# Kernel optimization log

Hardware: AMD Instinct MI355X
Metric: run time of the kernel (lower is better)

## Reference

```python
import jax, jax.numpy as jnp
import numpy as np

B = 128
N_ATOMS = 4096
NB, NA, NT = 4095, 4094, 4093
MAX_LEN = 5 * NT  # 20465, longest packed column (torsions)
EPS = 1e-8


def setup_inputs() -> dict:
    key = jax.random.key(0)
    ks = jax.random.split(key, 24)
    feats = jnp.zeros((B, MAX_LEN, 9), jnp.float32)
    # col 0: atom type ids
    atoms = jax.random.randint(ks[0], (B, N_ATOMS), 0, 6)
    # col 5: coords, flattened (N_ATOMS, 3)
    coords = jax.random.normal(ks[1], (B, N_ATOMS, 3), jnp.float32) * 5.0
    # col 6: bonds (i, j, type)
    bonds = jnp.stack([
        jax.random.randint(ks[2], (B, NB), 0, N_ATOMS),
        jax.random.randint(ks[3], (B, NB), 0, N_ATOMS),
        jax.random.randint(ks[4], (B, NB), 0, 15)], axis=-1)
    # col 7: angles (i, j, k, type)
    angles = jnp.stack([
        jax.random.randint(ks[5], (B, NA), 0, N_ATOMS),
        jax.random.randint(ks[6], (B, NA), 0, N_ATOMS),
        jax.random.randint(ks[7], (B, NA), 0, N_ATOMS),
        jax.random.randint(ks[8], (B, NA), 0, 13)], axis=-1)
    # col 8: torsions (i, j, k, l, type)
    tors = jnp.stack([
        jax.random.randint(ks[9], (B, NT), 0, N_ATOMS),
        jax.random.randint(ks[10], (B, NT), 0, N_ATOMS),
        jax.random.randint(ks[11], (B, NT), 0, N_ATOMS),
        jax.random.randint(ks[12], (B, NT), 0, N_ATOMS),
        jax.random.randint(ks[13], (B, NT), 0, 25)], axis=-1)
    feats = feats.at[:, :N_ATOMS, 0].set(atoms.astype(jnp.float32))
    feats = feats.at[:, :3 * N_ATOMS, 5].set(coords.reshape(B, -1))
    feats = feats.at[:, :3 * NB, 6].set(bonds.reshape(B, -1).astype(jnp.float32))
    feats = feats.at[:, :4 * NA, 7].set(angles.reshape(B, -1).astype(jnp.float32))
    feats = feats.at[:, :5 * NT, 8].set(tors.reshape(B, -1).astype(jnp.float32))
    lengths = jnp.tile(jnp.array(
        [[N_ATOMS, 0, 0, 0, 0, 3 * N_ATOMS, 3 * NB, 4 * NA, 5 * NT]],
        jnp.int32), (B, 1))
    bond_type = jnp.stack([jnp.ones(15), jax.random.uniform(ks[14], (15,), minval=1.0, maxval=2.0)], -1).astype(jnp.float32)
    angle_type = jnp.stack([jnp.ones(13), jax.random.uniform(ks[15], (13,), minval=1.0, maxval=3.0)], -1).astype(jnp.float32)
    tor_type = jnp.stack([jnp.ones(25), jax.random.uniform(ks[16], (25,), minval=0.0, maxval=3.14)], -1).astype(jnp.float32)
    multiplicity = jax.random.randint(ks[17], (25,), 1, 4)
    opt_pars = jax.random.uniform(ks[18], (47,), minval=0.5, maxval=1.5).astype(jnp.float32)
    return {"features": feats, "lengths": lengths, "bond_type": bond_type,
            "angle_type": angle_type, "tor_type": tor_type,
            "multiplicity": multiplicity, "opt_pars": opt_pars}


def _sample_energy(f, bond_type, angle_type, tor_type, multiplicity, opt_pars):
    coords = f[:3 * N_ATOMS, 5].reshape(-1, 3)                      # [N,3]
    bonds = f[:3 * NB, 6].astype(jnp.int32).reshape(-1, 3)          # [NB,3]
    angles = f[:4 * NA, 7].astype(jnp.int32).reshape(-1, 4)         # [NA,4]
    tors = f[:5 * NT, 8].astype(jnp.int32).reshape(-1, 5)           # [NT,5]

    # bonds: harmonic k*(r - r0)^2
    d = coords[bonds[:, 0]] - coords[bonds[:, 1]]
    r = jnp.sqrt(jnp.sum(d * d, -1) + EPS)
    pb = bond_type[bonds[:, 2]]
    e_bond = opt_pars[0] * jnp.sum(pb[:, 0] * (r - pb[:, 1]) ** 2)

    # angles: harmonic k*(theta - theta0)^2
    v1 = coords[angles[:, 0]] - coords[angles[:, 1]]
    v2 = coords[angles[:, 2]] - coords[angles[:, 1]]
    cosang = jnp.sum(v1 * v2, -1) / (
        jnp.sqrt(jnp.sum(v1 * v1, -1) + EPS) * jnp.sqrt(jnp.sum(v2 * v2, -1) + EPS))
    theta = jnp.arccos(jnp.clip(cosang, -1.0 + 1e-6, 1.0 - 1e-6))
    pa = angle_type[angles[:, 3]]
    e_ang = opt_pars[1] * jnp.sum(pa[:, 0] * (theta - pa[:, 1]) ** 2)

    # torsions: periodic k*(1 + cos(n*phi - delta))
    ci, cj, ck, cl = (coords[tors[:, m]] for m in range(4))
    b1, b2, b3 = cj - ci, ck - cj, cl - ck
    n1 = jnp.cross(b1, b2)
    n2 = jnp.cross(b2, b3)
    b2n = b2 / jnp.sqrt(jnp.sum(b2 * b2, -1, keepdims=True) + EPS)
    m1 = jnp.cross(n1, b2n)
    phi = jnp.arctan2(jnp.sum(m1 * n2, -1), jnp.sum(n1 * n2, -1))
    pt = tor_type[tors[:, 4]]
    n_mult = multiplicity[tors[:, 4]].astype(jnp.float32)
    e_tor = opt_pars[2] * jnp.sum(pt[:, 0] * (1.0 + jnp.cos(n_mult * phi - pt[:, 1])))

    return jnp.stack([e_bond, e_ang, e_tor])


def reference(features, lengths, bond_type, angle_type, tor_type, multiplicity, opt_pars):
    # lengths are uniform across batch (constants above); vmap over batch dim
    return jax.vmap(_sample_energy, in_axes=(0, None, None, None, None, None))(
        features, bond_type, angle_type, tor_type, multiplicity, opt_pars)
```

## Files before the change

### kernel.cpp

```cpp
#include <hip/hip_runtime.h>
#include <math.h>

#define BATCH    128
#define N_ATOMS  4096
#define NB       4095
#define NA       4094
#define NT       4093
#define FSTRIDE  184185
#define ROWS     20465
#define CROWS    12288
#define BROWS    12285
#define AROWS    16376
#define EPSV     1e-8f
#define THREADS  1024
#define WAVES    16
#define TPR      120

typedef float float4a __attribute__((ext_vector_type(4), aligned(4)));

__global__ __launch_bounds__(THREADS, 1) void
local_energy_v11(const float* __restrict__ F,
                 const float* __restrict__ bond_type,
                 const float* __restrict__ angle_type,
                 const float* __restrict__ tor_type,
                 const int*   __restrict__ multiplicity,
                 const float* __restrict__ opt_pars,
                 float*       __restrict__ out)
{
    __shared__ float          scc[CROWS];
    __shared__ unsigned short sbB[BROWS + 1];
    __shared__ unsigned short sbA[AROWS];
    __shared__ unsigned short sbT[ROWS + 1];
    __shared__ float sbt[30], sat[26], stt[50], smu[25];
    __shared__ float sred[WAVES * 2];

    const int b   = blockIdx.x;
    const int x   = b & 7;
    const int g   = b >> 3;
    const int s   = (g & 15) * 8 + x;
    const int p   = g >> 4;
    const int tid = threadIdx.x;
    const int w   = tid >> 6;
    const int l   = tid & 63;
    const size_t sbase = (size_t)s * FSTRIDE;

    if (tid < 30)                      sbt[tid]       = bond_type[tid];
    else if (tid >= 32 && tid < 58)    sat[tid - 32]  = angle_type[tid - 32];
    else if (tid >= 64 && tid < 114)   stt[tid - 64]  = tor_type[tid - 64];
    else if (tid >= 128 && tid < 153)  smu[tid - 128] = (float)multiplicity[tid - 128];

    const int tmax = p ? 137 : 171;
    for (int t = w; t < tmax; t += WAVES) {
        const int R0 = TPR * t + 2 * l;
        const int R1 = R0 + 1;
        float4a v0, v1;
        const bool ok0 = (R0 < ROWS);
        const bool ok1 = (R1 < ROWS);
        if (ok0) v0 = *(const float4a*)(F + sbase + (size_t)9 * R0 + 5);
        if (ok1) v1 = *(const float4a*)(F + sbase + (size_t)9 * R1 + 5);

        if (R1 < CROWS) {
            float2 c2; c2.x = v0.x; c2.y = v1.x;
            *(float2*)(scc + R0) = c2;
        }
        if (p) {
            if (R1 < BROWS) {
                unsigned pk = (unsigned)(unsigned short)(int)v0.y
                            | ((unsigned)(unsigned short)(int)v1.y << 16);
                *(unsigned*)(sbB + R0) = pk;
            } else if (R0 < BROWS) {
                sbB[R0] = (unsigned short)(int)v0.y;
            }
            if (R1 < AROWS) {
                unsigned pk = (unsigned)(unsigned short)(int)v0.z
                            | ((unsigned)(unsigned short)(int)v1.z << 16);
                *(unsigned*)(sbA + R0) = pk;
            }
        } else {
            if (ok1) {
                unsigned pk = (unsigned)(unsigned short)(int)v0.w
                            | ((unsigned)(unsigned short)(int)v1.w << 16);
                *(unsigned*)(sbT + R0) = pk;
            } else if (ok0) {
                sbT[R0] = (unsigned short)(int)v0.w;
            }
        }
    }
    __syncthreads();

    float eA = 0.f, eB = 0.f;
    if (p) {
        for (int i = tid; i < NB; i += THREADS) {
            const int a0 = sbB[3 * i + 0];
            const int a1 = sbB[3 * i + 1];
            const int bt = sbB[3 * i + 2];
            const float dx = scc[3 * a0 + 0] - scc[3 * a1 + 0];
            const float dy = scc[3 * a0 + 1] - scc[3 * a1 + 1];
            const float dz = scc[3 * a0 + 2] - scc[3 * a1 + 2];
            const float r  = sqrtf(dx * dx + dy * dy + dz * dz + EPSV);
            const float t0 = r - sbt[bt * 2 + 1];
            eA += sbt[bt * 2 + 0] * t0 * t0;
        }
        for (int i = tid; i < NA; i += THREADS) {
            const int a0 = sbA[4 * i + 0];
            const int a1 = sbA[4 * i + 1];
            const int a2 = sbA[4 * i + 2];
            const int at = sbA[4 * i + 3];
            const float v1x = scc[3 * a0 + 0] - scc[3 * a1 + 0];
            const float v1y = scc[3 * a0 + 1] - scc[3 * a1 + 1];
            const float v1z = scc[3 * a0 + 2] - scc[3 * a1 + 2];
            const float v2x = scc[3 * a2 + 0] - scc[3 * a1 + 0];
            const float v2y = scc[3 * a2 + 1] - scc[3 * a1 + 1];
            const float v2z = scc[3 * a2 + 2] - scc[3 * a1 + 2];
            const float d12 = v1x * v2x + v1y * v2y + v1z * v2z;
            const float n1  = sqrtf(v1x * v1x + v1y * v1y + v1z * v1z + EPSV);
            const float n2  = sqrtf(v2x * v2x + v2y * v2y + v2z * v2z + EPSV);
            float cosang = d12 / (n1 * n2);
            cosang = fminf(fmaxf(cosang, -1.0f + 1e-6f), 1.0f - 1e-6f);
            const float t0 = acosf(cosang) - sat[at * 2 + 1];
            eB += sat[at * 2 + 0] * t0 * t0;
        }
    } else {
        for (int i = tid; i < NT; i += THREADS) {
            const int ai = sbT[5 * i + 0];
            const int aj = sbT[5 * i + 1];
            const int ak = sbT[5 * i + 2];
            const int al = sbT[5 * i + 3];
            const int tt = sbT[5 * i + 4];
            const float b1x = scc[3*aj+0] - scc[3*ai+0];
            const float b1y = scc[3*aj+1] - scc[3*ai+1];
            const float b1z = scc[3*aj+2] - scc[3*ai+2];
            const float b2x = scc[3*ak+0] - scc[3*aj+0];
            const float b2y = scc[3*ak+1] - scc[3*aj+1];
            const float b2z = scc[3*ak+2] - scc[3*aj+2];
            const float b3x = scc[3*al+0] - scc[3*ak+0];
            const float b3y = scc[3*al+1] - scc[3*ak+1];
            const float b3z = scc[3*al+2] - scc[3*ak+2];
            const float n1x = b1y*b2z - b1z*b2y;
            const float n1y = b1z*b2x - b1x*b2z;
            const float n1z = b1x*b2y - b1y*b2x;
            const float n2x = b2y*b3z - b2z*b3y;
            const float n2y = b2z*b3x - b2x*b3z;
            const float n2z = b2x*b3y - b2y*b3x;
            const float inv = 1.0f / sqrtf(b2x*b2x + b2y*b2y + b2z*b2z + EPSV);
            const float bnx = b2x * inv, bny = b2y * inv, bnz = b2z * inv;
            const float m1x = n1y*bnz - n1z*bny;
            const float m1y = n1z*bnx - n1x*bnz;
            const float m1z = n1x*bny - n1y*bnx;
            const float phi = atan2f(m1x*n2x + m1y*n2y + m1z*n2z,
                                     n1x*n2x + n1y*n2y + n1z*n2z);
            eA += stt[tt * 2 + 0] * (1.0f + cosf(smu[tt] * phi - stt[tt * 2 + 1]));
        }
    }

    for (int off = 32; off > 0; off >>= 1) {
        eA += __shfl_down(eA, off);
        eB += __shfl_down(eB, off);
    }
    if (l == 0) {
        sred[w * 2 + 0] = eA;
        sred[w * 2 + 1] = eB;
    }
    __syncthreads();
    if (tid == 0) {
        float rA = 0.f, rB = 0.f;
        for (int i = 0; i < WAVES; ++i) { rA += sred[i * 2]; rB += sred[i * 2 + 1]; }
        if (p) {
            out[s * 3 + 0] = opt_pars[0] * rA;
            out[s * 3 + 1] = opt_pars[1] * rB;
        } else {
            out[s * 3 + 2] = opt_pars[2] * rA;
        }
    }
}

extern "C" void kernel_launch(void* const* d_in, const int* in_sizes, int n_in,
                              void* d_out, int out_size, void* d_ws, size_t ws_size,
                              hipStream_t stream) {
    const float* F            = (const float*)d_in[0];
    const float* bond_type    = (const float*)d_in[2];
    const float* angle_type   = (const float*)d_in[3];
    const float* tor_type     = (const float*)d_in[4];
    const int*   multiplicity = (const int*)  d_in[5];
    const float* opt_pars     = (const float*)d_in[6];
    float* out = (float*)d_out;

    local_energy_v11<<<dim3(BATCH * 2), dim3(THREADS), 0, stream>>>(
        F, bond_type, angle_type, tor_type, multiplicity, opt_pars, out);
}
```

Measured before the change: 154.1 us.

## Split feature loading between block pairs and exchange via workspace with grid sync

Adds a cooperative kernel in which each pair of blocks per sample loads a disjoint half of the sample's packed feature rows. The loads are contiguous, coalesced float4 chunks rather than the strided per-row reads used before. Each block scatters its columns into LDS, writes the part its partner needs to a global workspace, syncs the whole grid, and reads the partner's data back before computing bond/angle or torsion energies. This removes the duplicated read of coordinates and the strided access pattern, at the cost of a grid-wide barrier, an extra global round trip, and a dependence on the cooperative launch and workspace being available, with the old kernel kept as a fallback.

```diff
diff --git a/kernel.cpp b/kernel.cpp
--- a/kernel.cpp
+++ b/kernel.cpp
@@ -1,5 +1,8 @@
 #include <hip/hip_runtime.h>
+#include <hip/hip_cooperative_groups.h>
 #include <math.h>
+
+namespace cg = cooperative_groups;
 
 #define BATCH    128
 #define N_ATOMS  4096
@@ -16,7 +19,254 @@
 #define WAVES    16
 #define TPR      120
 
+#define NCHUNK_FULL 46046
+#define HCHUNK      23023
+#define SPLIT_ROW   10232
+
+#define OFF_SCC  0
+#define OFF_B    49152
+#define OFF_A    73728
+#define OFF_T    106480
+#define OFF_SBT  147412
+#define OFF_SAT  147532
+#define OFF_STT  147636
+#define OFF_SMU  147836
+#define OFF_SRED 147936
+#define OFF_D4   148128
+#define OFF_D2   148132
+#define LDS_SZ   148160
+
+#define WC       0
+#define WT       12288
+#define WB       17404
+#define WA       18432
+#define WSLOT    21504
+#define WS_NEED  ((size_t)WSLOT * 4 * BATCH)
+
 typedef float float4a __attribute__((ext_vector_type(4), aligned(4)));
+
+
+__device__ __forceinline__ float sel4f(const float4a v, const int e) {
+    float r = v.w;
+    r = (e == 0) ? v.x : r;
+    r = (e == 1) ? v.y : r;
+    r = (e == 2) ? v.z : r;
+    return r;
+}
+
+__device__ __forceinline__ void extract_chunk(char* __restrict__ lds,
+                                              const float4a v,
+                                              const int r0, const int c0) {
+    {
+        const float cv = sel4f(v, 5 - c0);
+        const bool  ok = ((unsigned)(5 - c0) < 4u) && (r0 < CROWS);
+        const int   ad = ok ? (OFF_SCC + (r0 << 2)) : OFF_D4;
+        *(float*)(lds + ad) = cv;
+    }
+    {
+        const int  iv = (int)sel4f(v, 6 - c0);
+        const bool ok = ((unsigned)(6 - c0) < 4u) && (r0 < BROWS);
+        const int  ad = ok ? (OFF_B + (r0 << 1)) : OFF_D2;
+        *(unsigned short*)(lds + ad) = (unsigned short)iv;
+    }
+    {
+        const int  iv = (int)sel4f(v, 7 - c0);
+        const bool ok = ((unsigned)(7 - c0) < 4u) && (r0 < AROWS);
+        const int  ad = ok ? (OFF_A + (r0 << 1)) : OFF_D2;
+        *(unsigned short*)(lds + ad) = (unsigned short)iv;
+    }
+    {
+        const int  iv = (int)sel4f(v, 8 - c0);
+        const bool ok = ((unsigned)(8 - c0) < 4u);
+        const int  ad = ok ? (OFF_T + (r0 << 1)) : OFF_D2;
+        *(unsigned short*)(lds + ad) = (unsigned short)iv;
+    }
+}
+
+__global__ __launch_bounds__(THREADS, 1) void
+local_energy_v16(const float* __restrict__ F,
+                 const float* __restrict__ bond_type,
+                 const float* __restrict__ angle_type,
+                 const float* __restrict__ tor_type,
+                 const int*   __restrict__ multiplicity,
+                 const float* __restrict__ opt_pars,
+                 unsigned*    __restrict__ ws,
+                 float*       __restrict__ out)
+{
+    __shared__ __align__(16) char LDSM[LDS_SZ];
+    char* lds = LDSM;
+
+    const int b   = blockIdx.x;
+    const int s   = b >> 1;
+    const int h   = b & 1;
+    const int tid = threadIdx.x;
+    const int w   = tid >> 6;
+    const int l   = tid & 63;
+    const float* Fb = F + (size_t)s * FSTRIDE;
+
+    float* sbt = (float*)(lds + OFF_SBT);
+    float* sat = (float*)(lds + OFF_SAT);
+    float* stt = (float*)(lds + OFF_STT);
+    float* smu = (float*)(lds + OFF_SMU);
+    float* srd = (float*)(lds + OFF_SRED);
+
+    if (tid < 30)                      sbt[tid]       = bond_type[tid];
+    else if (tid >= 32 && tid < 58)    sat[tid - 32]  = angle_type[tid - 32];
+    else if (tid >= 64 && tid < 114)   stt[tid - 64]  = tor_type[tid - 64];
+    else if (tid >= 128 && tid < 153)  smu[tid - 128] = (float)multiplicity[tid - 128];
+
+    const int cbase = h ? HCHUNK : 0;
+    {
+        const int f0i = 4 * (cbase + tid);
+        int r0 = f0i / 9;
+        int c0 = f0i - 9 * r0;
+
+        for (int j = 0; j < 22; j += 2) {
+            const int ci0 = cbase + tid + (j << 10);
+            const float4a v0 = *(const float4a*)(Fb + 4 * ci0);
+            const float4a v1 = *(const float4a*)(Fb + 4 * ci0 + 4096);
+            extract_chunk(lds, v0, r0, c0);
+            { c0 += 1; r0 += 455; if (c0 == 9) { c0 = 0; r0 += 1; } }
+            extract_chunk(lds, v1, r0, c0);
+            { c0 += 1; r0 += 455; if (c0 == 9) { c0 = 0; r0 += 1; } }
+        }
+        if (tid < 495) {
+            const int ci = cbase + tid + (22 << 10);
+            const float4a v = *(const float4a*)(Fb + 4 * ci);
+            extract_chunk(lds, v, r0, c0);
+        } else if (h && tid == 495) {
+            const float x = Fb[FSTRIDE - 1];
+            *(unsigned short*)(lds + OFF_T + (20464 << 1)) = (unsigned short)(int)x;
+        }
+    }
+    __syncthreads();
+
+    unsigned* W = ws + (size_t)s * WSLOT;
+    if (h == 0) {
+        const unsigned* sC = (const unsigned*)(lds + OFF_SCC);
+        for (int i = tid; i < 10232; i += THREADS) W[WC + i] = sC[i];
+        const unsigned* sT = (const unsigned*)(lds + OFF_T);
+        for (int i = tid; i < 5116; i += THREADS) W[WT + i] = sT[i];
+    } else {
+        const unsigned* sC = (const unsigned*)(lds + OFF_SCC);
+        for (int i = tid; i < 2056; i += THREADS) W[WC + SPLIT_ROW + i] = sC[SPLIT_ROW + i];
+        const unsigned* sB = (const unsigned*)(lds + OFF_B);
+        for (int i = tid; i < 1027; i += THREADS) W[WB + i] = sB[5116 + i];
+        const unsigned* sA = (const unsigned*)(lds + OFF_A);
+        for (int i = tid; i < 3072; i += THREADS) W[WA + i] = sA[5116 + i];
+    }
+
+    __threadfence();
+    cg::this_grid().sync();
+    __threadfence();
+
+    if (h == 0) {
+        unsigned* dC = (unsigned*)(lds + OFF_SCC);
+        for (int i = tid; i < 2056; i += THREADS) dC[SPLIT_ROW + i] = W[WC + SPLIT_ROW + i];
+        unsigned* dB = (unsigned*)(lds + OFF_B);
+        for (int i = tid; i < 1027; i += THREADS) dB[5116 + i] = W[WB + i];
+        unsigned* dA = (unsigned*)(lds + OFF_A);
+        for (int i = tid; i < 3072; i += THREADS) dA[5116 + i] = W[WA + i];
+    } else {
+        unsigned* dC = (unsigned*)(lds + OFF_SCC);
+        for (int i = tid; i < 10232; i += THREADS) dC[i] = W[WC + i];
+        unsigned* dT = (unsigned*)(lds + OFF_T);
+        for (int i = tid; i < 5116; i += THREADS) dT[i] = W[WT + i];
+    }
+    __syncthreads();
+
+    const float*          scc = (const float*)(lds + OFF_SCC);
+    const unsigned short* pB  = (const unsigned short*)(lds + OFF_B);
+    const unsigned short* pA  = (const unsigned short*)(lds + OFF_A);
+    const unsigned short* pT  = (const unsigned short*)(lds + OFF_T);
+
+    float eA = 0.f, eB = 0.f;
+    if (h == 0) {
+        for (int i = tid; i < NB; i += THREADS) {
+            const int a0 = pB[3 * i + 0];
+            const int a1 = pB[3 * i + 1];
+            const int bt = pB[3 * i + 2];
+            const float dx = scc[3 * a0 + 0] - scc[3 * a1 + 0];
+            const float dy = scc[3 * a0 + 1] - scc[3 * a1 + 1];
+            const float dz = scc[3 * a0 + 2] - scc[3 * a1 + 2];
+            const float r  = sqrtf(dx * dx + dy * dy + dz * dz + EPSV);
+            const float t0 = r - sbt[bt * 2 + 1];
+            eA += sbt[bt * 2 + 0] * t0 * t0;
+        }
+        for (int i = tid; i < NA; i += THREADS) {
+            const int a0 = pA[4 * i + 0];
+            const int a1 = pA[4 * i + 1];
+            const int a2 = pA[4 * i + 2];
+            const int at = pA[4 * i + 3];
+            const float v1x = scc[3 * a0 + 0] - scc[3 * a1 + 0];
+            const float v1y = scc[3 * a0 + 1] - scc[3 * a1 + 1];
+            const float v1z = scc[3 * a0 + 2] - scc[3 * a1 + 2];
+            const float v2x = scc[3 * a2 + 0] - scc[3 * a1 + 0];
+            const float v2y = scc[3 * a2 + 1] - scc[3 * a1 + 1];
+            const float v2z = scc[3 * a2 + 2] - scc[3 * a1 + 2];
+            const float d12 = v1x * v2x + v1y * v2y + v1z * v2z;
+            const float n1  = sqrtf(v1x * v1x + v1y * v1y + v1z * v1z + EPSV);
+            const float n2  = sqrtf(v2x * v2x + v2y * v2y + v2z * v2z + EPSV);
+            float cosang = d12 / (n1 * n2);
+            cosang = fminf(fmaxf(cosang, -1.0f + 1e-6f), 1.0f - 1e-6f);
+            const float t0 = acosf(cosang) - sat[at * 2 + 1];
+            eB += sat[at * 2 + 0] * t0 * t0;
+        }
+    } else {
+        for (int i = tid; i < NT; i += THREADS) {
+            const int ai = pT[5 * i + 0];
+            const int aj = pT[5 * i + 1];
+            const int ak = pT[5 * i + 2];
+            const int al = pT[5 * i + 3];
+            const int tt = pT[5 * i + 4];
+            const float b1x = scc[3*aj+0] - scc[3*ai+0];
+            const float b1y = scc[3*aj+1] - scc[3*ai+1];
+            const float b1z = scc[3*aj+2] - scc[3*ai+2];
+            const float b2x = scc[3*ak+0] - scc[3*aj+0];
+            const float b2y = scc[3*ak+1] - scc[3*aj+1];
+            const float b2z = scc[3*ak+2] - scc[3*aj+2];
+            const float b3x = scc[3*al+0] - scc[3*ak+0];
+            const float b3y = scc[3*al+1] - scc[3*ak+1];
+            const float b3z = scc[3*al+2] - scc[3*ak+2];
+            const float n1x = b1y*b2z - b1z*b2y;
+            const float n1y = b1z*b2x - b1x*b2z;
+            const float n1z = b1x*b2y - b1y*b2x;
+            const float n2x = b2y*b3z - b2z*b3y;
+            const float n2y = b2z*b3x - b2x*b3z;
+            const float n2z = b2x*b3y - b2y*b3x;
+            const float inv = 1.0f / sqrtf(b2x*b2x + b2y*b2y + b2z*b2z + EPSV);
+            const float bnx = b2x * inv, bny = b2y * inv, bnz = b2z * inv;
+            const float m1x = n1y*bnz - n1z*bny;
+            const float m1y = n1z*bnx - n1x*bnz;
+            const float m1z = n1x*bny - n1y*bnx;
+            const float phi = atan2f(m1x*n2x + m1y*n2y + m1z*n2z,
+                                     n1x*n2x + n1y*n2y + n1z*n2z);
+            eA += stt[tt * 2 + 0] * (1.0f + cosf(smu[tt] * phi - stt[tt * 2 + 1]));
+        }
+    }
+
+    for (int off = 32; off > 0; off >>= 1) {
+        eA += __shfl_down(eA, off);
+        eB += __shfl_down(eB, off);
+    }
+    if (l == 0) {
+        srd[w * 2 + 0] = eA;
+        srd[w * 2 + 1] = eB;
+    }
+    __syncthreads();
+    if (tid == 0) {
+        float rA = 0.f, rB = 0.f;
+        for (int i = 0; i < WAVES; ++i) { rA += srd[i * 2]; rB += srd[i * 2 + 1]; }
+        if (h == 0) {
+            out[s * 3 + 0] = opt_pars[0] * rA;
+            out[s * 3 + 1] = opt_pars[1] * rB;
+        } else {
+            out[s * 3 + 2] = opt_pars[2] * rA;
+        }
+    }
+}
+
+typedef float float4f __attribute__((ext_vector_type(4), aligned(4)));
 
 __global__ __launch_bounds__(THREADS, 1) void
 local_energy_v11(const float* __restrict__ F,
@@ -53,12 +303,11 @@
     for (int t = w; t < tmax; t += WAVES) {
         const int R0 = TPR * t + 2 * l;
         const int R1 = R0 + 1;
-        float4a v0, v1;
+        float4f v0, v1;
         const bool ok0 = (R0 < ROWS);
         const bool ok1 = (R1 < ROWS);
-        if (ok0) v0 = *(const float4a*)(F + sbase + (size_t)9 * R0 + 5);
-        if (ok1) v1 = *(const float4a*)(F + sbase + (size_t)9 * R1 + 5);
-
+        if (ok0) v0 = *(const float4f*)(F + sbase + (size_t)9 * R0 + 5);
+        if (ok1) v1 = *(const float4f*)(F + sbase + (size_t)9 * R1 + 5);
         if (R1 < CROWS) {
             float2 c2; c2.x = v0.x; c2.y = v1.x;
             *(float2*)(scc + R0) = c2;
@@ -183,8 +432,19 @@
     const float* tor_type     = (const float*)d_in[4];
     const int*   multiplicity = (const int*)  d_in[5];
     const float* opt_pars     = (const float*)d_in[6];
-    float* out = (float*)d_out;
-
+    float*       out          = (float*)d_out;
+    unsigned*    wsp          = (unsigned*)d_ws;
+
+    if (d_ws != nullptr && ws_size >= WS_NEED) {
+        void* args[] = { (void*)&F, (void*)&bond_type, (void*)&angle_type,
+                         (void*)&tor_type, (void*)&multiplicity,
+                         (void*)&opt_pars, (void*)&wsp, (void*)&out };
+        hipError_t e = hipLaunchCooperativeKernel(
+            reinterpret_cast<void*>(local_energy_v16),
+            dim3(BATCH * 2), dim3(THREADS), args, 0, stream);
+        if (e == hipSuccess) return;
+        (void)hipGetLastError();
+    }
     local_energy_v11<<<dim3(BATCH * 2), dim3(THREADS), 0, stream>>>(
         F, bond_type, angle_type, tor_type, multiplicity, opt_pars, out);
 }
```

Result: slower. 347.7 us (+125.7%).

## Overlap bond and torsion compute with tail of global staging loads

Applied to the files above, without the earlier changes.

Splits the staging loop into a head phase that loads coordinates and the early index rows, then a tail phase. During the tail, global loads for the remaining angle or torsion rows are issued while already-staged bonds and the first torsions are evaluated. The aim is to hide global memory latency behind compute instead of serialising load then compute. It adds an extra barrier and relies on hard-coded cut points (HEAD_T, CUT_T) being consistent with which rows are already in shared memory.

```diff
diff --git a/kernel.cpp b/kernel.cpp
--- a/kernel.cpp
+++ b/kernel.cpp
@@ -15,11 +15,66 @@
 #define THREADS  1024
 #define WAVES    16
 #define TPR      120
+#define HEAD_T   103
+#define CUT_T    2472
 
 typedef float float4a __attribute__((ext_vector_type(4), aligned(4)));
 
+
+__device__ __forceinline__ float bond_term(const int i,
+        const unsigned short* __restrict__ sbB,
+        const float* __restrict__ scc,
+        const float* __restrict__ sbt)
+{
+    const int a0 = sbB[3 * i + 0];
+    const int a1 = sbB[3 * i + 1];
+    const int bt = sbB[3 * i + 2];
+    const float dx = scc[3 * a0 + 0] - scc[3 * a1 + 0];
+    const float dy = scc[3 * a0 + 1] - scc[3 * a1 + 1];
+    const float dz = scc[3 * a0 + 2] - scc[3 * a1 + 2];
+    const float r  = sqrtf(dx * dx + dy * dy + dz * dz + EPSV);
+    const float t0 = r - sbt[bt * 2 + 1];
+    return sbt[bt * 2 + 0] * t0 * t0;
+}
+
+__device__ __forceinline__ float tor_term(const int i,
+        const unsigned short* __restrict__ sbT,
+        const float* __restrict__ scc,
+        const float* __restrict__ stt,
+        const float* __restrict__ smu)
+{
+    const int ai = sbT[5 * i + 0];
+    const int aj = sbT[5 * i + 1];
+    const int ak = sbT[5 * i + 2];
+    const int al = sbT[5 * i + 3];
+    const int tt = sbT[5 * i + 4];
+    const float b1x = scc[3*aj+0] - scc[3*ai+0];
+    const float b1y = scc[3*aj+1] - scc[3*ai+1];
+    const float b1z = scc[3*aj+2] - scc[3*ai+2];
+    const float b2x = scc[3*ak+0] - scc[3*aj+0];
+    const float b2y = scc[3*ak+1] - scc[3*aj+1];
+    const float b2z = scc[3*ak+2] - scc[3*aj+2];
+    const float b3x = scc[3*al+0] - scc[3*ak+0];
+    const float b3y = scc[3*al+1] - scc[3*ak+1];
+    const float b3z = scc[3*al+2] - scc[3*ak+2];
+    const float n1x = b1y*b2z - b1z*b2y;
+    const float n1y = b1z*b2x - b1x*b2z;
+    const float n1z = b1x*b2y - b1y*b2x;
+    const float n2x = b2y*b3z - b2z*b3y;
+    const float n2y = b2z*b3x - b2x*b3z;
+    const float n2z = b2x*b3y - b2y*b3x;
+    const float inv = 1.0f / sqrtf(b2x*b2x + b2y*b2y + b2z*b2z + EPSV);
+    const float bnx = b2x * inv, bny = b2y * inv, bnz = b2z * inv;
+    const float m1x = n1y*bnz - n1z*bny;
+    const float m1y = n1z*bnx - n1x*bnz;
+    const float m1z = n1x*bny - n1y*bnx;
+    const float phi = atan2f(m1x*n2x + m1y*n2y + m1z*n2z,
+                             n1x*n2x + n1y*n2y + n1z*n2z);
+    return stt[tt * 2 + 0] * (1.0f + cosf(smu[tt] * phi - stt[tt * 2 + 1]));
+}
+
 __global__ __launch_bounds__(THREADS, 1) void
-local_energy_v11(const float* __restrict__ F,
+local_energy_v17(const float* __restrict__ F,
                  const float* __restrict__ bond_type,
                  const float* __restrict__ angle_type,
                  const float* __restrict__ tor_type,
@@ -49,15 +104,13 @@
     else if (tid >= 64 && tid < 114)   stt[tid - 64]  = tor_type[tid - 64];
     else if (tid >= 128 && tid < 153)  smu[tid - 128] = (float)multiplicity[tid - 128];
 
-    const int tmax = p ? 137 : 171;
-    for (int t = w; t < tmax; t += WAVES) {
+    float eA = 0.f, eB = 0.f;
+
+    for (int t = w; t < HEAD_T; t += WAVES) {
         const int R0 = TPR * t + 2 * l;
         const int R1 = R0 + 1;
-        float4a v0, v1;
-        const bool ok0 = (R0 < ROWS);
-        const bool ok1 = (R1 < ROWS);
-        if (ok0) v0 = *(const float4a*)(F + sbase + (size_t)9 * R0 + 5);
-        if (ok1) v1 = *(const float4a*)(F + sbase + (size_t)9 * R1 + 5);
+        const float4a v0 = *(const float4a*)(F + sbase + (size_t)9 * R0 + 5);
+        const float4a v1 = *(const float4a*)(F + sbase + (size_t)9 * R1 + 5);
 
         if (R1 < CROWS) {
             float2 c2; c2.x = v0.x; c2.y = v1.x;
@@ -71,36 +124,46 @@
             } else if (R0 < BROWS) {
                 sbB[R0] = (unsigned short)(int)v0.y;
             }
+            {
+                unsigned pk = (unsigned)(unsigned short)(int)v0.z
+                            | ((unsigned)(unsigned short)(int)v1.z << 16);
+                *(unsigned*)(sbA + R0) = pk;
+            }
+        } else {
+            {
+                unsigned pk = (unsigned)(unsigned short)(int)v0.w
+                            | ((unsigned)(unsigned short)(int)v1.w << 16);
+                *(unsigned*)(sbT + R0) = pk;
+            }
+        }
+    }
+    __syncthreads();
+
+    if (p) {
+        int q = 0;
+        for (int t = HEAD_T + w; t < 137; t += WAVES) {
+            const int R0 = TPR * t + 2 * l;
+            const int R1 = R0 + 1;
+            const float4a v0 = *(const float4a*)(F + sbase + (size_t)9 * R0 + 5);
+            const float4a v1 = *(const float4a*)(F + sbase + (size_t)9 * R1 + 5);
+
+            if (q == 0) {
+                eA += bond_term(tid, sbB, scc, sbt);
+                eA += bond_term(tid + 1024, sbB, scc, sbt);
+            } else if (q == 1) {
+                eA += bond_term(tid + 2048, sbB, scc, sbt);
+                if (tid + 3072 < NB) eA += bond_term(tid + 3072, sbB, scc, sbt);
+            }
+            ++q;
+
             if (R1 < AROWS) {
                 unsigned pk = (unsigned)(unsigned short)(int)v0.z
                             | ((unsigned)(unsigned short)(int)v1.z << 16);
                 *(unsigned*)(sbA + R0) = pk;
             }
-        } else {
-            if (ok1) {
-                unsigned pk = (unsigned)(unsigned short)(int)v0.w
-                            | ((unsigned)(unsigned short)(int)v1.w << 16);
-                *(unsigned*)(sbT + R0) = pk;
-            } else if (ok0) {
-                sbT[R0] = (unsigned short)(int)v0.w;
-            }
-        }
-    }
-    __syncthreads();
-
-    float eA = 0.f, eB = 0.f;
-    if (p) {
-        for (int i = tid; i < NB; i += THREADS) {
-            const int a0 = sbB[3 * i + 0];
-            const int a1 = sbB[3 * i + 1];
-            const int bt = sbB[3 * i + 2];
-            const float dx = scc[3 * a0 + 0] - scc[3 * a1 + 0];
-            const float dy = scc[3 * a0 + 1] - scc[3 * a1 + 1];
-            const float dz = scc[3 * a0 + 2] - scc[3 * a1 + 2];
-            const float r  = sqrtf(dx * dx + dy * dy + dz * dz + EPSV);
-            const float t0 = r - sbt[bt * 2 + 1];
-            eA += sbt[bt * 2 + 0] * t0 * t0;
-        }
+        }
+        __syncthreads();
+
         for (int i = tid; i < NA; i += THREADS) {
             const int a0 = sbA[4 * i + 0];
             const int a1 = sbA[4 * i + 1];
@@ -121,36 +184,34 @@
             eB += sat[at * 2 + 0] * t0 * t0;
         }
     } else {
-        for (int i = tid; i < NT; i += THREADS) {
-            const int ai = sbT[5 * i + 0];
-            const int aj = sbT[5 * i + 1];
-            const int ak = sbT[5 * i + 2];
-            const int al = sbT[5 * i + 3];
-            const int tt = sbT[5 * i + 4];
-            const float b1x = scc[3*aj+0] - scc[3*ai+0];
-            const float b1y = scc[3*aj+1] - scc[3*ai+1];
-            const float b1z = scc[3*aj+2] - scc[3*ai+2];
-            const float b2x = scc[3*ak+0] - scc[3*aj+0];
-            const float b2y = scc[3*ak+1] - scc[3*aj+1];
-            const float b2z = scc[3*ak+2] - scc[3*aj+2];
-            const float b3x = scc[3*al+0] - scc[3*ak+0];
-            const float b3y = scc[3*al+1] - scc[3*ak+1];
-            const float b3z = scc[3*al+2] - scc[3*ak+2];
-            const float n1x = b1y*b2z - b1z*b2y;
-            const float n1y = b1z*b2x - b1x*b2z;
-            const float n1z = b1x*b2y - b1y*b2x;
-            const float n2x = b2y*b3z - b2z*b3y;
-            const float n2y = b2z*b3x - b2x*b3z;
-            const float n2z = b2x*b3y - b2y*b3x;
-            const float inv = 1.0f / sqrtf(b2x*b2x + b2y*b2y + b2z*b2z + EPSV);
-            const float bnx = b2x * inv, bny = b2y * inv, bnz = b2z * inv;
-            const float m1x = n1y*bnz - n1z*bny;
-            const float m1y = n1z*bnx - n1x*bnz;
-            const float m1z = n1x*bny - n1y*bnx;
-            const float phi = atan2f(m1x*n2x + m1y*n2y + m1z*n2z,
-                                     n1x*n2x + n1y*n2y + n1z*n2z);
-            eA += stt[tt * 2 + 0] * (1.0f + cosf(smu[tt] * phi - stt[tt * 2 + 1]));
-        }
+        int q = 0;
+        for (int t = HEAD_T + w; t < 171; t += WAVES) {
+            const int R0 = TPR * t + 2 * l;
+            const int R1 = R0 + 1;
+            float4a v0, v1;
+            const bool ok0 = (R0 < ROWS);
+            const bool ok1 = (R1 < ROWS);
+            if (ok0) v0 = *(const float4a*)(F + sbase + (size_t)9 * R0 + 5);
+            if (ok1) v1 = *(const float4a*)(F + sbase + (size_t)9 * R1 + 5);
+
+            if (q < 3) {
+                const int i = tid + (q << 10);
+                if (i < CUT_T) eA += tor_term(i, sbT, scc, stt, smu);
+            }
+            ++q;
+
+            if (ok1) {
+                unsigned pk = (unsigned)(unsigned short)(int)v0.w
+                            | ((unsigned)(unsigned short)(int)v1.w << 16);
+                *(unsigned*)(sbT + R0) = pk;
+            } else if (ok0) {
+                sbT[R0] = (unsigned short)(int)v0.w;
+            }
+        }
+        __syncthreads();
+
+        for (int i = tid; i < NT; i += THREADS)
+            if (i >= CUT_T) eA += tor_term(i, sbT, scc, stt, smu);
     }
 
     for (int off = 32; off > 0; off >>= 1) {
@@ -185,6 +246,6 @@
     const float* opt_pars     = (const float*)d_in[6];
     float* out = (float*)d_out;
 
-    local_energy_v11<<<dim3(BATCH * 2), dim3(THREADS), 0, stream>>>(
+    local_energy_v17<<<dim3(BATCH * 2), dim3(THREADS), 0, stream>>>(
         F, bond_type, angle_type, tor_type, multiplicity, opt_pars, out);
 }
```

Result: no change. 156.1 us (+1.3%).
